# Optimization experiments

Hardware: AMD Instinct MI355X
Metric: run time of the kernel (lower is better)

## Reference

```python
import jax, jax.numpy as jnp
import numpy as np

N = 100000      # nodes
E = 1600000     # edges (avg degree 16)
F_IN = 64       # num_features
HID = 16        # hidden channels (fixed in module)
OUT = 32        # num_classes
K = 2           # kernel_size (dim=1, degree=1 open B-spline -> 2 basis fns)


def setup_inputs() -> dict:
    key = jax.random.key(0)
    ks = jax.random.split(key, 8)
    return {
        "x": jax.random.normal(ks[0], (N, F_IN), jnp.float32),
        "edge_index": jax.random.randint(ks[1], (2, E), 0, N, dtype=jnp.int64),
        "dropout": 0,  # unused in eval mode (F.dropout training=False)
        "edge_attr": jnp.full((E, 1), 0.1, jnp.float32),  # nt([0.1]) broadcast per edge
        "W1": jax.random.normal(ks[2], (K, F_IN, HID), jnp.float32) / np.sqrt(K * F_IN).astype(np.float32),
        "root1": jax.random.normal(ks[3], (F_IN, HID), jnp.float32) / np.sqrt(F_IN).astype(np.float32),
        "bias1": jnp.zeros((HID,), jnp.float32),
        "W2": jax.random.normal(ks[4], (K, HID, OUT), jnp.float32) / np.sqrt(K * HID).astype(np.float32),
        "root2": jax.random.normal(ks[5], (HID, OUT), jnp.float32) / np.sqrt(HID).astype(np.float32),
        "bias2": jnp.zeros((OUT,), jnp.float32),
    }


def spline_conv(x, edge_index, edge_attr, W, root, bias):
    """SplineConv, dim=1, kernel_size=2, degree=1 open B-spline, aggr='mean'."""
    src, dst = edge_index[0], edge_index[1]
    n = x.shape[0]
    u = edge_attr[:, 0]                                  # [E] pseudo-coords in [0,1]
    # degree-1 open spline, kernel_size=2: frac = u*(ks-1) = u; kernels {0,1}
    basis = jnp.stack([1.0 - u, u], axis=1)              # [E, K]
    # transform at node level (cheaper than gathering raw features per edge)
    h = jnp.einsum('nf,kfo->nko', x, W)                  # [N, K, out]
    msg = jnp.einsum('ek,eko->eo', basis, h[src])        # [E, out]
    summed = jax.ops.segment_sum(msg, dst, num_segments=n)
    deg = jax.ops.segment_sum(jnp.ones_like(u), dst, num_segments=n)
    out = summed / jnp.maximum(deg, 1.0)[:, None]        # mean aggregation
    return out + x @ root + bias                          # root weight + bias


def reference(x, edge_index, dropout, edge_attr, W1, root1, bias1, W2, root2, bias2):
    # dropout is a no-op in eval mode
    h = jax.nn.elu(spline_conv(x, edge_index, edge_attr, W1, root1, bias1))
    h = spline_conv(h, edge_index, edge_attr, W2, root2, bias2)
    return jax.nn.log_softmax(h, axis=1)
```

## Files before the change

kernel.cpp:

```cpp
#include <hip/hip_runtime.h>
#include <math.h>

#define NN 100000
#define NE 1600000
#define F_IN 64
#define HID 16
#define OUTF 32
#define BKT_SHIFT 6
#define BKT_NODES 64
#define NBKT 1563
#define SRCM 0x1FFFF
#define CAP_REG 2048
#define CAP_LDS 1536
#define PBLK2 256
#define EPB2 (NE / PBLK2)
#define OVF_MAX 4096

__device__ __forceinline__ unsigned bf16r(float f) {
    unsigned u = __float_as_uint(f);
    return (u + 0x7FFFu + ((u >> 16) & 1u)) >> 16;
}
__device__ __forceinline__ float bfa(unsigned p) { return __uint_as_float(p << 16); }
__device__ __forceinline__ float bfd(unsigned p) { return __uint_as_float(p & 0xFFFF0000u); }

__global__ __launch_bounds__(1024) void partF_kernel(const int* __restrict__ ei,
                                                     const float* __restrict__ ea,
                                                     int* __restrict__ gcur,
                                                     int* __restrict__ novf,
                                                     int4* __restrict__ ovf,
                                                     int2* __restrict__ bkt) {
    __shared__ int hcnt[NBKT];
    __shared__ int hbase[NBKT];
    int t = threadIdx.x, blk = blockIdx.x;
    for (int i = t; i < NBKT; i += 1024) hcnt[i] = 0;
    __syncthreads();
    int beg = blk * EPB2, end = beg + EPB2;
    for (int e = beg + t; e < end; e += 1024)
        atomicAdd(&hcnt[ei[NE + e] >> BKT_SHIFT], 1);
    __syncthreads();
    for (int i = t; i < NBKT; i += 1024) {
        int c = hcnt[i];
        hbase[i] = c ? atomicAdd(&gcur[i], c) : 0;
        hcnt[i] = 0;
    }
    __syncthreads();
    for (int e = beg + t; e < end; e += 1024) {
        int src = ei[e];
        int dst = ei[NE + e];
        float u = ea[e];
        int b = dst >> BKT_SHIFT;
        int r = atomicAdd(&hcnt[b], 1);
        int pos = hbase[b] + r;
        int pay = src | ((dst & (BKT_NODES - 1)) << 17);
        if (pos < CAP_REG) {
            bkt[(size_t)b * CAP_REG + pos] = make_int2(pay, __float_as_int(u));
        } else {
            int o = atomicAdd(novf, 1);
            if (o < OVF_MAX) ovf[o] = make_int4(dst, src, __float_as_int(u), 0);
        }
    }
}

__global__ __launch_bounds__(256) void proj1_kernel(const float* __restrict__ x,
                                                    const float* __restrict__ W1,
                                                    const float* __restrict__ root1,
                                                    const float* __restrict__ bias1,
                                                    unsigned* __restrict__ ab1p,
                                                    float* __restrict__ r1) {
    __shared__ float w[2 * F_IN * HID];
    __shared__ float wr[F_IN * HID];
    __shared__ float bb[HID];
    for (int i = threadIdx.x; i < 2 * F_IN * HID; i += 256) w[i] = W1[i];
    for (int i = threadIdx.x; i < F_IN * HID; i += 256) wr[i] = root1[i];
    if (threadIdx.x < HID) bb[threadIdx.x] = bias1[threadIdx.x];
    __syncthreads();
    int n = blockIdx.x * 256 + threadIdx.x;
    if (n >= NN) return;
    float accA[HID], accB[HID], accR[HID];
#pragma unroll
    for (int o = 0; o < HID; ++o) { accA[o] = 0.f; accB[o] = 0.f; accR[o] = bb[o]; }
    const float* xr = x + (size_t)n * F_IN;
    for (int f = 0; f < F_IN; ++f) {
        float xv = xr[f];
        const float* w0 = &w[f * HID];
        const float* w1 = &w[F_IN * HID + f * HID];
        const float* w2 = &wr[f * HID];
#pragma unroll
        for (int o = 0; o < HID; ++o) {
            accA[o] = fmaf(xv, w0[o], accA[o]);
            accB[o] = fmaf(xv, w1[o], accB[o]);
            accR[o] = fmaf(xv, w2[o], accR[o]);
        }
    }
    unsigned* ar = ab1p + (size_t)n * HID;
    float* rr = r1 + (size_t)n * HID;
#pragma unroll
    for (int o = 0; o < HID; ++o) {
        ar[o] = bf16r(accA[o]) | (bf16r(accB[o] - accA[o]) << 16);
        rr[o] = accR[o];
    }
}

__global__ __launch_bounds__(512) void gather1_kernel(const int* __restrict__ gcur,
                                                      const int* __restrict__ novf,
                                                      const int4* __restrict__ ovf,
                                                      const int2* __restrict__ bkt,
                                                      const unsigned* __restrict__ ab1p,
                                                      const float* __restrict__ r1,
                                                      unsigned short* __restrict__ h16,
                                                      float* __restrict__ dinv) {
    __shared__ int2 sorted[CAP_LDS];
    __shared__ int cnt[BKT_NODES], cur[BKT_NODES], segb[BKT_NODES + 1];
    __shared__ float accL[BKT_NODES * HID];
    __shared__ float degsL[BKT_NODES];
    int t = threadIdx.x;
    int b = blockIdx.x;
    int tot = gcur[b];
    int beg = b * CAP_REG;
    if (t < BKT_NODES) { cnt[t] = 0; cur[t] = 0; degsL[t] = 0.f; }
    __syncthreads();
    int nodeBase = b * BKT_NODES;

    if (tot <= CAP_LDS) {
        int end = beg + tot;
        for (int e = beg + t; e < end; e += 512)
            atomicAdd(&cnt[((unsigned)bkt[e].x) >> 17], 1);
        __syncthreads();
        if (t < BKT_NODES) {
            int v = cnt[t];
            int sc = v;
#pragma unroll
            for (int off = 1; off < 64; off <<= 1) {
                int o = __shfl_up(sc, off, 64);
                if (t >= off) sc += o;
            }
            segb[t] = sc - v;
            if (t == 63) segb[64] = sc;
        }
        __syncthreads();
        for (int e = beg + t; e < end; e += 512) {
            int2 pk = bkt[e];
            int loc = ((unsigned)pk.x) >> 17;
            int pos = segb[loc] + atomicAdd(&cur[loc], 1);
            sorted[pos] = pk;
        }
        __syncthreads();
        int j = t & (HID - 1);
        int g = t >> 4;
        int s = segb[2 * g], mid = segb[2 * g + 1], e2 = segb[2 * g + 2];
        float a0 = 0.f, a1 = 0.f;
        int e = s;
        for (; e + 8 <= e2; e += 8) {
            float val[8]; int sel[8];
#pragma unroll
            for (int k = 0; k < 8; ++k) {
                int2 pk = sorted[e + k];
                unsigned p = ab1p[(size_t)(pk.x & SRCM) * HID + j];
                val[k] = fmaf(__int_as_float(pk.y), bfd(p), bfa(p));
                sel[k] = (e + k) >= mid;
            }
#pragma unroll
            for (int k = 0; k < 8; ++k) {
                a0 += sel[k] ? 0.f : val[k];
                a1 += sel[k] ? val[k] : 0.f;
            }
        }
        for (; e < e2; ++e) {
            int2 pk = sorted[e];
            unsigned p = ab1p[(size_t)(pk.x & SRCM) * HID + j];
            float val = fmaf(__int_as_float(pk.y), bfd(p), bfa(p));
            if (e >= mid) a1 += val; else a0 += val;
        }
        float d0 = 1.f / (float)max(mid - s, 1);
        float d1 = 1.f / (float)max(e2 - mid, 1);
        int n0 = nodeBase + 2 * g, n1 = n0 + 1;
        if (n0 < NN) {
            float v = a0 * d0 + r1[(size_t)n0 * HID + j];
            h16[(size_t)n0 * HID + j] = (unsigned short)bf16r(v > 0.f ? v : expm1f(v));
            if (j == 0) dinv[n0] = d0;
        }
        if (n1 < NN) {
            float v = a1 * d1 + r1[(size_t)n1 * HID + j];
            h16[(size_t)n1 * HID + j] = (unsigned short)bf16r(v > 0.f ? v : expm1f(v));
            if (j == 0) dinv[n1] = d1;
        }
    } else {
        int inreg = min(tot, CAP_REG);
        int end = beg + inreg;
        for (int i = t; i < BKT_NODES * HID; i += 512) accL[i] = 0.f;
        __syncthreads();
        int j = t & (HID - 1);
        int g = t >> 4;
        for (int e = beg + g; e < end; e += 32) {
            int2 pk = bkt[e];
            unsigned p = ab1p[(size_t)(pk.x & SRCM) * HID + j];
            atomicAdd(&accL[(((unsigned)pk.x) >> 17) * HID + j],
                      fmaf(__int_as_float(pk.y), bfd(p), bfa(p)));
            if (j == 0) atomicAdd(&degsL[((unsigned)pk.x) >> 17], 1.f);
        }
        int ovn = min(novf[0], OVF_MAX);
        for (int o = 0; o < ovn; ++o) {
            int4 ent = ovf[o];
            int loc = ent.x - nodeBase;
            if (loc >= 0 && loc < BKT_NODES && g == 0) {
                unsigned p = ab1p[(size_t)ent.y * HID + j];
                atomicAdd(&accL[loc * HID + j], fmaf(__int_as_float(ent.z), bfd(p), bfa(p)));
                if (j == 0) atomicAdd(&degsL[loc], 1.f);
            }
        }
        __syncthreads();
        if (t < BKT_NODES) degsL[t] = 1.f / fmaxf(degsL[t], 1.f);
        __syncthreads();
#pragma unroll
        for (int it = 0; it < BKT_NODES * HID / 512; ++it) {
            int idx = it * 512 + t;
            int nl = idx >> 4, jj = idx & (HID - 1);
            int n = nodeBase + nl;
            if (n < NN) {
                float v = accL[idx] * degsL[nl] + r1[(size_t)n * HID + jj];
                h16[(size_t)n * HID + jj] = (unsigned short)bf16r(v > 0.f ? v : expm1f(v));
            }
        }
        if (t < BKT_NODES && nodeBase + t < NN) dinv[nodeBase + t] = degsL[t];
    }
}

__global__ __launch_bounds__(512) void gather2_kernel(const int* __restrict__ gcur,
                                                      const int* __restrict__ novf,
                                                      const int4* __restrict__ ovf,
                                                      const int2* __restrict__ bkt,
                                                      const unsigned short* __restrict__ h16,
                                                      const float* __restrict__ W2,
                                                      const float* __restrict__ root2,
                                                      const float* __restrict__ bias2,
                                                      const float* __restrict__ dinv,
                                                      float* __restrict__ out) {
    __shared__ int2 sorted[CAP_LDS];
    __shared__ int cnt[BKT_NODES], cur[BKT_NODES], segb[BKT_NODES + 1];
    __shared__ float s0L[BKT_NODES * HID];
    __shared__ float s1L[BKT_NODES * HID];
    __shared__ float w20[HID * OUTF], w2d[HID * OUTF], wr[HID * OUTF];
    __shared__ float bb[OUTF];
    int t = threadIdx.x;
    for (int i = t; i < HID * OUTF; i += 512) {
        float a = W2[i];
        w20[i] = a;
        w2d[i] = W2[HID * OUTF + i] - a;
        wr[i] = root2[i];
    }
    if (t < OUTF) bb[t] = bias2[t];
    if (t < BKT_NODES) { cnt[t] = 0; cur[t] = 0; }
    int b = blockIdx.x;
    int tot = gcur[b];
    int beg = b * CAP_REG;
    int nodeBase = b * BKT_NODES;
    __syncthreads();

    if (tot <= CAP_LDS) {
        int end = beg + tot;
        for (int e = beg + t; e < end; e += 512)
            atomicAdd(&cnt[((unsigned)bkt[e].x) >> 17], 1);
        __syncthreads();
        if (t < BKT_NODES) {
            int v = cnt[t];
            int sc = v;
#pragma unroll
            for (int off = 1; off < 64; off <<= 1) {
                int o = __shfl_up(sc, off, 64);
                if (t >= off) sc += o;
            }
            segb[t] = sc - v;
            if (t == 63) segb[64] = sc;
        }
        __syncthreads();
        for (int e = beg + t; e < end; e += 512) {
            int2 pk = bkt[e];
            int loc = ((unsigned)pk.x) >> 17;
            int pos = segb[loc] + atomicAdd(&cur[loc], 1);
            sorted[pos] = pk;
        }
        __syncthreads();
        int j = t & (HID - 1);
        int g = t >> 4;
        int s = segb[2 * g], mid = segb[2 * g + 1], e2 = segb[2 * g + 2];
        float s00 = 0.f, s10 = 0.f, s01 = 0.f, s11 = 0.f;
        int e = s;
        for (; e + 8 <= e2; e += 8) {
            float hv[8], uv[8]; int sel[8];
#pragma unroll
            for (int k = 0; k < 8; ++k) {
                int2 pk = sorted[e + k];
                hv[k] = __uint_as_float(((unsigned)h16[(size_t)(pk.x & SRCM) * HID + j]) << 16);
                uv[k] = __int_as_float(pk.y);
                sel[k] = (e + k) >= mid;
            }
#pragma unroll
            for (int k = 0; k < 8; ++k) {
                float uh = uv[k] * hv[k];
                s00 += sel[k] ? 0.f : hv[k];
                s10 += sel[k] ? 0.f : uh;
                s01 += sel[k] ? hv[k] : 0.f;
                s11 += sel[k] ? uh : 0.f;
            }
        }
        for (; e < e2; ++e) {
            int2 pk = sorted[e];
            float hvv = __uint_as_float(((unsigned)h16[(size_t)(pk.x & SRCM) * HID + j]) << 16);
            float uh = __int_as_float(pk.y) * hvv;
            if (e >= mid) { s01 += hvv; s11 += uh; }
            else          { s00 += hvv; s10 += uh; }
        }
        s0L[(2 * g) * HID + j] = s00;
        s1L[(2 * g) * HID + j] = s10;
        s0L[(2 * g + 1) * HID + j] = s01;
        s1L[(2 * g + 1) * HID + j] = s11;
        __syncthreads();
    } else {
        int inreg = min(tot, CAP_REG);
        int end = beg + inreg;
        for (int i = t; i < BKT_NODES * HID; i += 512) { s0L[i] = 0.f; s1L[i] = 0.f; }
        __syncthreads();
        int j = t & (HID - 1);
        int g = t >> 4;
        for (int e = beg + g; e < end; e += 32) {
            int2 pk = bkt[e];
            float hvv = __uint_as_float(((unsigned)h16[(size_t)(pk.x & SRCM) * HID + j]) << 16);
            int l = ((unsigned)pk.x) >> 17;
            atomicAdd(&s0L[l * HID + j], hvv);
            atomicAdd(&s1L[l * HID + j], __int_as_float(pk.y) * hvv);
        }
        int ovn = min(novf[0], OVF_MAX);
        for (int o = 0; o < ovn; ++o) {
            int4 ent = ovf[o];
            int loc = ent.x - nodeBase;
            if (loc >= 0 && loc < BKT_NODES && g == 0) {
                float hvv = __uint_as_float(((unsigned)h16[(size_t)ent.y * HID + j]) << 16);
                atomicAdd(&s0L[loc * HID + j], hvv);
                atomicAdd(&s1L[loc * HID + j], __int_as_float(ent.z) * hvv);
            }
        }
        __syncthreads();
    }

#pragma unroll
    for (int it = 0; it < BKT_NODES * OUTF / 512; ++it) {
        int idx = it * 512 + t;
        int nl = idx >> 5, jj = idx & (OUTF - 1);
        int n = nodeBase + nl;
        float v = 0.f;
        if (n < NN) {
            float msum = 0.f;
            const float* S0 = &s0L[nl * HID];
            const float* S1 = &s1L[nl * HID];
#pragma unroll
            for (int f = 0; f < HID; ++f)
                msum += S0[f] * w20[f * OUTF + jj] + S1[f] * w2d[f * OUTF + jj];
            v = msum * dinv[n] + bb[jj];
            const unsigned short* hr = h16 + (size_t)n * HID;
#pragma unroll
            for (int f = 0; f < HID; ++f)
                v = fmaf(__uint_as_float(((unsigned)hr[f]) << 16), wr[f * OUTF + jj], v);
        }
        float m = v;
#pragma unroll
        for (int mask = 16; mask >= 1; mask >>= 1) m = fmaxf(m, __shfl_xor(m, mask));
        float ex = expf(v - m);
        float sm = ex;
#pragma unroll
        for (int mask = 16; mask >= 1; mask >>= 1) sm += __shfl_xor(sm, mask);
        if (n < NN) out[(size_t)n * OUTF + jj] = v - m - logf(sm);
    }
}

extern "C" void kernel_launch(void* const* d_in, const int* in_sizes, int n_in,
                              void* d_out, int out_size, void* d_ws, size_t ws_size,
                              hipStream_t stream) {
    const float* x     = (const float*)d_in[0];
    const int*   ei    = (const int*)d_in[1];
    const float* ea    = (const float*)d_in[3];
    const float* W1    = (const float*)d_in[4];
    const float* root1 = (const float*)d_in[5];
    const float* bias1 = (const float*)d_in[6];
    const float* W2    = (const float*)d_in[7];
    const float* root2 = (const float*)d_in[8];
    const float* bias2 = (const float*)d_in[9];
    float* out = (float*)d_out;
    float* ws  = (float*)d_ws;

    const size_t N = NN;
    int*            gcur = (int*)(ws);
    int*            novf = (int*)(ws + 2000);
    int4*           ovf  = (int4*)(ws + 2048);
    float*          dinv = ws + 20000;
    float*          r1   = ws + 120000;
    unsigned*       ab1p = (unsigned*)(ws + 120000 + 16 * N);
    unsigned short* h16  = (unsigned short*)(ws + 120000 + 32 * N);
    int2*           bkt  = (int2*)(ws + 120000 + 40 * N);

    hipMemsetAsync(gcur, 0, 8448, stream);

    int nbN = (NN + 255) / 256;
    partF_kernel<<<PBLK2, 1024, 0, stream>>>(ei, ea, gcur, novf, ovf, bkt);
    proj1_kernel<<<nbN, 256, 0, stream>>>(x, W1, root1, bias1, ab1p, r1);
    gather1_kernel<<<NBKT, 512, 0, stream>>>(gcur, novf, ovf, bkt, ab1p, r1, h16, dinv);
    gather2_kernel<<<NBKT, 512, 0, stream>>>(gcur, novf, ovf, bkt, h16, W2, root2, bias2, dinv, out);
}
```

Baseline: 128.8 us.

## Stage partition scatter in LDS and reuse sorted buckets in second gather

```diff
diff --git a/kernel.cpp b/kernel.cpp
--- a/kernel.cpp
+++ b/kernel.cpp
@@ -12,7 +12,7 @@
 #define SRCM 0x1FFFF
 #define CAP_REG 2048
 #define CAP_LDS 1536
-#define PBLK2 256
+#define PBLK2 512
 #define EPB2 (NE / PBLK2)
 #define OVF_MAX 4096
 
@@ -22,6 +22,7 @@
 }
 __device__ __forceinline__ float bfa(unsigned p) { return __uint_as_float(p << 16); }
 __device__ __forceinline__ float bfd(unsigned p) { return __uint_as_float(p & 0xFFFF0000u); }
+__device__ __forceinline__ float bfh(unsigned short v) { return __uint_as_float(((unsigned)v) << 16); }
 
 __global__ __launch_bounds__(1024) void partF_kernel(const int* __restrict__ ei,
                                                      const float* __restrict__ ea,
@@ -31,12 +32,31 @@
                                                      int2* __restrict__ bkt) {
     __shared__ int hcnt[NBKT];
     __shared__ int hbase[NBKT];
+    __shared__ int lbase[NBKT];
+    __shared__ int s[1024];
+    __shared__ int2 sbuf[EPB2];
+    __shared__ unsigned short bid[EPB2];
     int t = threadIdx.x, blk = blockIdx.x;
     for (int i = t; i < NBKT; i += 1024) hcnt[i] = 0;
     __syncthreads();
     int beg = blk * EPB2, end = beg + EPB2;
     for (int e = beg + t; e < end; e += 1024)
         atomicAdd(&hcnt[ei[NE + e] >> BKT_SHIFT], 1);
+    __syncthreads();
+    int i0 = 2 * t, i1 = 2 * t + 1;
+    int v0 = (i0 < NBKT) ? hcnt[i0] : 0;
+    int v1 = (i1 < NBKT) ? hcnt[i1] : 0;
+    s[t] = v0 + v1;
+    __syncthreads();
+    for (int off = 1; off < 1024; off <<= 1) {
+        int xv = (t >= off) ? s[t - off] : 0;
+        __syncthreads();
+        s[t] += xv;
+        __syncthreads();
+    }
+    int run = (t == 0) ? 0 : s[t - 1];
+    if (i0 < NBKT) lbase[i0] = run;
+    if (i1 < NBKT) lbase[i1] = run + v0;
     __syncthreads();
     for (int i = t; i < NBKT; i += 1024) {
         int c = hcnt[i];
@@ -50,13 +70,21 @@
         float u = ea[e];
         int b = dst >> BKT_SHIFT;
         int r = atomicAdd(&hcnt[b], 1);
-        int pos = hbase[b] + r;
-        int pay = src | ((dst & (BKT_NODES - 1)) << 17);
-        if (pos < CAP_REG) {
-            bkt[(size_t)b * CAP_REG + pos] = make_int2(pay, __float_as_int(u));
+        int lp = lbase[b] + r;
+        sbuf[lp] = make_int2(src | ((dst & (BKT_NODES - 1)) << 17), __float_as_int(u));
+        bid[lp] = (unsigned short)b;
+    }
+    __syncthreads();
+    for (int i = t; i < EPB2; i += 1024) {
+        int2 pk = sbuf[i];
+        int b = bid[i];
+        int p = hbase[b] + (i - lbase[b]);
+        if (p < CAP_REG) {
+            bkt[(size_t)b * CAP_REG + p] = pk;
         } else {
             int o = atomicAdd(novf, 1);
-            if (o < OVF_MAX) ovf[o] = make_int4(dst, src, __float_as_int(u), 0);
+            if (o < OVF_MAX)
+                ovf[o] = make_int4(b * BKT_NODES + (pk.x >> 17), pk.x & SRCM, pk.y, 0);
         }
     }
 }
@@ -104,11 +132,12 @@
 __global__ __launch_bounds__(512) void gather1_kernel(const int* __restrict__ gcur,
                                                       const int* __restrict__ novf,
                                                       const int4* __restrict__ ovf,
-                                                      const int2* __restrict__ bkt,
+                                                      int2* __restrict__ bkt,
                                                       const unsigned* __restrict__ ab1p,
                                                       const float* __restrict__ r1,
                                                       unsigned short* __restrict__ h16,
-                                                      float* __restrict__ dinv) {
+                                                      float* __restrict__ dinv,
+                                                      int* __restrict__ segg) {
     __shared__ int2 sorted[CAP_LDS];
     __shared__ int cnt[BKT_NODES], cur[BKT_NODES], segb[BKT_NODES + 1];
     __shared__ float accL[BKT_NODES * HID];
@@ -145,6 +174,8 @@
             sorted[pos] = pk;
         }
         __syncthreads();
+        for (int e = t; e < tot; e += 512) bkt[beg + e] = sorted[e];
+        if (t <= BKT_NODES) segg[b * (BKT_NODES + 1) + t] = segb[t];
         int j = t & (HID - 1);
         int g = t >> 4;
         int s = segb[2 * g], mid = segb[2 * g + 1], e2 = segb[2 * g + 2];
@@ -234,9 +265,9 @@
                                                       const float* __restrict__ root2,
                                                       const float* __restrict__ bias2,
                                                       const float* __restrict__ dinv,
+                                                      const int* __restrict__ segg,
                                                       float* __restrict__ out) {
-    __shared__ int2 sorted[CAP_LDS];
-    __shared__ int cnt[BKT_NODES], cur[BKT_NODES], segb[BKT_NODES + 1];
+    __shared__ int segb[BKT_NODES + 1];
     __shared__ float s0L[BKT_NODES * HID];
     __shared__ float s1L[BKT_NODES * HID];
     __shared__ float w20[HID * OUTF], w2d[HID * OUTF], wr[HID * OUTF];
@@ -249,37 +280,15 @@
         wr[i] = root2[i];
     }
     if (t < OUTF) bb[t] = bias2[t];
-    if (t < BKT_NODES) { cnt[t] = 0; cur[t] = 0; }
     int b = blockIdx.x;
     int tot = gcur[b];
     int beg = b * CAP_REG;
     int nodeBase = b * BKT_NODES;
+    if (t <= BKT_NODES) segb[t] = segg[b * (BKT_NODES + 1) + t];
     __syncthreads();
 
     if (tot <= CAP_LDS) {
-        int end = beg + tot;
-        for (int e = beg + t; e < end; e += 512)
-            atomicAdd(&cnt[((unsigned)bkt[e].x) >> 17], 1);
-        __syncthreads();
-        if (t < BKT_NODES) {
-            int v = cnt[t];
-            int sc = v;
-#pragma unroll
-            for (int off = 1; off < 64; off <<= 1) {
-                int o = __shfl_up(sc, off, 64);
-                if (t >= off) sc += o;
-            }
-            segb[t] = sc - v;
-            if (t == 63) segb[64] = sc;
-        }
-        __syncthreads();
-        for (int e = beg + t; e < end; e += 512) {
-            int2 pk = bkt[e];
-            int loc = ((unsigned)pk.x) >> 17;
-            int pos = segb[loc] + atomicAdd(&cur[loc], 1);
-            sorted[pos] = pk;
-        }
-        __syncthreads();
+        const int2* sp = bkt + beg;
         int j = t & (HID - 1);
         int g = t >> 4;
         int s = segb[2 * g], mid = segb[2 * g + 1], e2 = segb[2 * g + 2];
@@ -289,8 +298,8 @@
             float hv[8], uv[8]; int sel[8];
 #pragma unroll
             for (int k = 0; k < 8; ++k) {
-                int2 pk = sorted[e + k];
-                hv[k] = __uint_as_float(((unsigned)h16[(size_t)(pk.x & SRCM) * HID + j]) << 16);
+                int2 pk = sp[e + k];
+                hv[k] = bfh(h16[(size_t)(pk.x & SRCM) * HID + j]);
                 uv[k] = __int_as_float(pk.y);
                 sel[k] = (e + k) >= mid;
             }
@@ -304,8 +313,8 @@
             }
         }
         for (; e < e2; ++e) {
-            int2 pk = sorted[e];
-            float hvv = __uint_as_float(((unsigned)h16[(size_t)(pk.x & SRCM) * HID + j]) << 16);
+            int2 pk = sp[e];
+            float hvv = bfh(h16[(size_t)(pk.x & SRCM) * HID + j]);
             float uh = __int_as_float(pk.y) * hvv;
             if (e >= mid) { s01 += hvv; s11 += uh; }
             else          { s00 += hvv; s10 += uh; }
@@ -324,7 +333,7 @@
         int g = t >> 4;
         for (int e = beg + g; e < end; e += 32) {
             int2 pk = bkt[e];
-            float hvv = __uint_as_float(((unsigned)h16[(size_t)(pk.x & SRCM) * HID + j]) << 16);
+            float hvv = bfh(h16[(size_t)(pk.x & SRCM) * HID + j]);
             int l = ((unsigned)pk.x) >> 17;
             atomicAdd(&s0L[l * HID + j], hvv);
             atomicAdd(&s1L[l * HID + j], __int_as_float(pk.y) * hvv);
@@ -334,7 +343,7 @@
             int4 ent = ovf[o];
             int loc = ent.x - nodeBase;
             if (loc >= 0 && loc < BKT_NODES && g == 0) {
-                float hvv = __uint_as_float(((unsigned)h16[(size_t)ent.y * HID + j]) << 16);
+                float hvv = bfh(h16[(size_t)ent.y * HID + j]);
                 atomicAdd(&s0L[loc * HID + j], hvv);
                 atomicAdd(&s1L[loc * HID + j], __int_as_float(ent.z) * hvv);
             }
@@ -359,7 +368,7 @@
             const unsigned short* hr = h16 + (size_t)n * HID;
 #pragma unroll
             for (int f = 0; f < HID; ++f)
-                v = fmaf(__uint_as_float(((unsigned)hr[f]) << 16), wr[f * OUTF + jj], v);
+                v = fmaf(bfh(hr[f]), wr[f * OUTF + jj], v);
         }
         float m = v;
 #pragma unroll
@@ -392,16 +401,17 @@
     int*            novf = (int*)(ws + 2000);
     int4*           ovf  = (int4*)(ws + 2048);
     float*          dinv = ws + 20000;
-    float*          r1   = ws + 120000;
-    unsigned*       ab1p = (unsigned*)(ws + 120000 + 16 * N);
-    unsigned short* h16  = (unsigned short*)(ws + 120000 + 32 * N);
-    int2*           bkt  = (int2*)(ws + 120000 + 40 * N);
+    int*            segg = (int*)(ws + 120000);
+    float*          r1   = ws + 222000;
+    unsigned*       ab1p = (unsigned*)(ws + 222000 + 16 * N);
+    unsigned short* h16  = (unsigned short*)(ws + 222000 + 32 * N);
+    int2*           bkt  = (int2*)(ws + 222000 + 40 * N);
 
     hipMemsetAsync(gcur, 0, 8448, stream);
 
     int nbN = (NN + 255) / 256;
     partF_kernel<<<PBLK2, 1024, 0, stream>>>(ei, ea, gcur, novf, ovf, bkt);
     proj1_kernel<<<nbN, 256, 0, stream>>>(x, W1, root1, bias1, ab1p, r1);
-    gather1_kernel<<<NBKT, 512, 0, stream>>>(gcur, novf, ovf, bkt, ab1p, r1, h16, dinv);
-    gather2_kernel<<<NBKT, 512, 0, stream>>>(gcur, novf, ovf, bkt, h16, W2, root2, bias2, dinv, out);
-}
+    gather1_kernel<<<NBKT, 512, 0, stream>>>(gcur, novf, ovf, bkt, ab1p, r1, h16, dinv, segg);
+    gather2_kernel<<<NBKT, 512, 0, stream>>>(gcur, novf, ovf, bkt, h16, W2, root2, bias2, dinv, segg, out);
+}
```

After: 138.1 us. 1.07x slower.
